# Kernel tuning notes

Hardware: AMD Instinct MI355X
Metric: run time of the kernel (lower is better)

## Reference

```python
import jax, jax.numpy as jnp
import numpy as np

N = 10000      # number of keypoints / graph nodes
CIN = 512      # in_channels
COUT = 512     # out_channels
KCHEB = 5      # Chebyshev order K
KNN = 20       # k nearest neighbors


def setup_inputs() -> dict:
    key = jax.random.key(0)
    k1, k2, k3, k4 = jax.random.split(key, 4)
    x = jax.random.normal(k1, (1, CIN, N), dtype=jnp.float32)
    position = jax.random.normal(k2, (1, N, 3), dtype=jnp.float32)
    # ChebConv weights: one [CIN, COUT] matrix per Chebyshev order, plus bias
    theta = jax.random.normal(k3, (KCHEB, CIN, COUT), dtype=jnp.float32) / np.float32(np.sqrt(CIN * KCHEB))
    bias = jax.random.normal(k4, (COUT,), dtype=jnp.float32) * 0.01
    return {"x": x, "position": position, "theta": theta, "bias": bias, "knn": KNN}


def reference(x, position, theta, bias, knn):
    # ---- knn_graph(position.squeeze(0), k, flow='target_to_source') ----
    pos = position[0]                       # [N, 3]
    n = pos.shape[0]
    sq = jnp.sum(pos * pos, axis=1)
    d2 = sq[:, None] + sq[None, :] - 2.0 * (pos @ pos.T)   # [N, N] squared dists
    d2 = jnp.where(jnp.eye(n, dtype=bool), jnp.inf, d2)    # exclude self (loop=False)
    _, nbr = jax.lax.top_k(-d2, knn)        # [N, knn] nearest neighbor indices
    # flow='target_to_source' => edge_index = [center, neighbor]
    row = jnp.repeat(jnp.arange(n), knn)    # edge source (center) for ChebConv
    col = nbr.reshape(-1)                   # edge target (neighbor)

    # ---- ChebConv sym normalization, lambda_max=2 => L_hat = -D^-1/2 A D^-1/2 ----
    deg = jnp.zeros((n,), x.dtype).at[row].add(jnp.float32(1.0))
    dis = jnp.where(deg > 0, jax.lax.rsqrt(deg), jnp.float32(0.0))
    w = -dis[row] * dis[col]                # [E] edge weights, zero diagonal

    h = jnp.swapaxes(x, 1, 2)               # [B, N, CIN]

    def prop(t):
        # out[target] += w * t[source]  (sparse L_hat @ t)
        msg = t[:, row, :] * w[None, :, None]
        return jnp.zeros_like(t).at[:, col, :].add(msg)

    # Chebyshev recurrence: Tx0 = h, Tx1 = L_hat h, Tx_k = 2 L_hat Tx_{k-1} - Tx_{k-2}
    Tx0 = h
    out = jnp.einsum('bnc,co->bno', Tx0, theta[0])
    Tx1 = prop(Tx0)
    out = out + jnp.einsum('bnc,co->bno', Tx1, theta[1])
    for k in range(2, theta.shape[0]):
        Tx2 = 2.0 * prop(Tx1) - Tx0
        out = out + jnp.einsum('bnc,co->bno', Tx2, theta[k])
        Tx0, Tx1 = Tx1, Tx2
    out = out + bias
    return jnp.swapaxes(out, 1, 2)          # [B, COUT, N]
```

## Files before the change

### kernel.cpp

```cpp
#include <hip/hip_runtime.h>
#include <hip/hip_bf16.h>
#include <cstdint>
#include <cstddef>

#define N_NODES 10000
#define KNN_K 20
#define NEDGE (N_NODES * KNN_K)
#define NBATCH 157
#define POS4_PAD 10048
#define NCELL 4096
#define NPX 1250

using bf16x8 = __attribute__((ext_vector_type(8))) short;
using f32x4  = __attribute__((ext_vector_type(4))) float;

__device__ __forceinline__ float bf_lo(unsigned int u) {
  union { unsigned int i; float f; } c; c.i = u << 16; return c.f;
}
__device__ __forceinline__ float bf_hi(unsigned int u) {
  union { unsigned int i; float f; } c; c.i = u & 0xFFFF0000u; return c.f;
}
__device__ __forceinline__ unsigned short f2bf(float f) {
  union { float f; unsigned int i; } c; c.f = f;
  unsigned int u = c.i;
  u += 0x7FFFu + ((u >> 16) & 1u);
  return (unsigned short)(u >> 16);
}

__device__ __forceinline__ void gll16(const void* g, void* l) {
  __builtin_amdgcn_global_load_lds(
      (const __attribute__((address_space(1))) unsigned int*)g,
      (__attribute__((address_space(3))) unsigned int*)l,
      16, 0, 0);
}

__global__ __launch_bounds__(256) void transpose_f32_bf16(
    const float* __restrict__ src0, unsigned short* __restrict__ dst,
    int srows, int scols, int dstride, size_t slice_elems, int dcol_per_slice)
{
  __shared__ float lds[64 * 65];
  const int z = blockIdx.z;
  const float* src = src0 + (size_t)z * slice_elems;
  const int dcol0 = z * dcol_per_slice;
  const int c0 = blockIdx.x * 64;
  const int r0 = blockIdx.y * 64;
  const int tid = threadIdx.x;
#pragma unroll
  for (int q = 0; q < 4; ++q) {
    int unit = q * 256 + tid;
    int rr = unit >> 4;
    int cu = unit & 15;
    int r = r0 + rr, c = c0 + cu * 4;
    float4 v = make_float4(0.f, 0.f, 0.f, 0.f);
    if (r < srows && c + 3 < scols) v = *(const float4*)&src[(size_t)r * scols + c];
    lds[rr * 65 + cu * 4 + 0] = v.x;
    lds[rr * 65 + cu * 4 + 1] = v.y;
    lds[rr * 65 + cu * 4 + 2] = v.z;
    lds[rr * 65 + cu * 4 + 3] = v.w;
  }
  __syncthreads();
#pragma unroll
  for (int q = 0; q < 2; ++q) {
    int unit = q * 256 + tid;
    int cl = unit >> 3;
    int ru = unit & 7;
    int c = c0 + cl;
    if (c < scols) {
      unsigned short tmp[8];
#pragma unroll
      for (int j = 0; j < 8; ++j) tmp[j] = f2bf(lds[(ru * 8 + j) * 65 + cl]);
      uint4 o;
      o.x = (unsigned int)tmp[0] | ((unsigned int)tmp[1] << 16);
      o.y = (unsigned int)tmp[2] | ((unsigned int)tmp[3] << 16);
      o.z = (unsigned int)tmp[4] | ((unsigned int)tmp[5] << 16);
      o.w = (unsigned int)tmp[6] | ((unsigned int)tmp[7] << 16);
      *(uint4*)&dst[(size_t)c * dstride + dcol0 + r0 + ru * 8] = o;
    }
  }
}

__global__ __launch_bounds__(256) void pos4_kernel(
    const float* __restrict__ pos, float4* __restrict__ pos4,
    int* __restrict__ counts, int* __restrict__ cursor,
    int* __restrict__ cellid, int* __restrict__ cellcnt,
    int* __restrict__ nfail)
{
  int c = blockIdx.x * 256 + threadIdx.x;
  if (c == 0) *nfail = 0;
  if (c < POS4_PAD) {
    float4 v;
    if (c < N_NODES) {
      float x = pos[c * 3 + 0], y = pos[c * 3 + 1], z = pos[c * 3 + 2];
      v = make_float4(x, y, z, x * x + y * y + z * z);
      int cx = min(15, max(0, (int)floorf((x + 4.0f) * 2.0f)));
      int cy = min(15, max(0, (int)floorf((y + 4.0f) * 2.0f)));
      int cz = min(15, max(0, (int)floorf((z + 4.0f) * 2.0f)));
      int cell = (cx << 8) | (cy << 4) | cz;
      cellid[c] = cell;
      atomicAdd(&cellcnt[cell], 1);
      counts[c] = 0; cursor[c] = 0;
    } else {
      v = make_float4(0.f, 0.f, 0.f, __builtin_inff());
    }
    pos4[c] = v;
  }
}

__global__ __launch_bounds__(256) void cellscan_kernel(
    const int* __restrict__ cellcnt, int* __restrict__ cellptr)
{
  __shared__ int part[256];
  const int tid = threadIdx.x;
  const int base = tid * 16;
  int cv[16];
  int s = 0;
#pragma unroll
  for (int q = 0; q < 4; ++q) {
    int4 v = *(const int4*)&cellcnt[base + q * 4];
    cv[q * 4 + 0] = v.x; cv[q * 4 + 1] = v.y;
    cv[q * 4 + 2] = v.z; cv[q * 4 + 3] = v.w;
    s += v.x + v.y + v.z + v.w;
  }
  part[tid] = s;
  __syncthreads();
  for (int off = 1; off < 256; off <<= 1) {
    int add = (tid >= off) ? part[tid - off] : 0;
    __syncthreads();
    part[tid] += add;
    __syncthreads();
  }
  int run = part[tid] - s;
#pragma unroll
  for (int q = 0; q < 16; ++q) { cellptr[base + q] = run; run += cv[q]; }
  if (tid == 255) cellptr[NCELL] = run;
}

__global__ __launch_bounds__(256) void perm_kernel(
    const int* __restrict__ cellid, const int* __restrict__ cellptr,
    int* __restrict__ cellcur, int* __restrict__ perm,
    const float4* __restrict__ pos4, float4* __restrict__ pos4s)
{
  int c = blockIdx.x * 256 + threadIdx.x;
  if (c < N_NODES) {
    int cell = cellid[c];
    int p = atomicAdd(&cellcur[cell], 1);
    int slot = cellptr[cell] + p;
    perm[slot] = c;
    pos4s[slot] = pos4[c];
  }
}

__device__ __forceinline__ float knn_dist(float4 pi, float4 s) {
  float dot = fmaf(pi.x, s.x, fmaf(pi.y, s.y, pi.z * s.z));
  return fmaf(-2.0f, dot, pi.w + s.w);
}

__device__ __forceinline__ void insert8(float r[8], float k) {
  asm("v_med3_f32 %0, %1, %2, %3" : "=v"(r[7]) : "v"(k), "v"(r[6]), "v"(r[7]));
  asm("v_med3_f32 %0, %1, %2, %3" : "=v"(r[6]) : "v"(k), "v"(r[5]), "v"(r[6]));
  asm("v_med3_f32 %0, %1, %2, %3" : "=v"(r[5]) : "v"(k), "v"(r[4]), "v"(r[5]));
  asm("v_med3_f32 %0, %1, %2, %3" : "=v"(r[4]) : "v"(k), "v"(r[3]), "v"(r[4]));
  asm("v_med3_f32 %0, %1, %2, %3" : "=v"(r[3]) : "v"(k), "v"(r[2]), "v"(r[3]));
  asm("v_med3_f32 %0, %1, %2, %3" : "=v"(r[2]) : "v"(k), "v"(r[1]), "v"(r[2]));
  asm("v_med3_f32 %0, %1, %2, %3" : "=v"(r[1]) : "v"(k), "v"(r[0]), "v"(r[1]));
  r[0] = fminf(r[0], k);
}

__device__ __forceinline__ float merge_tau20(float r[8], int lane) {
  const float INF = __builtin_inff();
  float tau = INF;
#pragma unroll
  for (int t = 0; t < KNN_K; ++t) {
    float m = r[0];
    m = fminf(m, __shfl_xor(m, 1));
    m = fminf(m, __shfl_xor(m, 2));
    m = fminf(m, __shfl_xor(m, 4));
    m = fminf(m, __shfl_xor(m, 8));
    m = fminf(m, __shfl_xor(m, 16));
    m = fminf(m, __shfl_xor(m, 32));
    unsigned long long who = __ballot(r[0] == m);
    int srcl = __ffsll(who) - 1;
    if (lane == srcl) {
#pragma unroll
      for (int z = 0; z < 7; ++z) r[z] = r[z + 1];
      r[7] = INF;
    }
    tau = m;
  }
  return tau;
}

__device__ __forceinline__ void emit_hits(
    int i, bool valid, float d, float tau, int cid, int lane, int& cnt,
    int* __restrict__ knn_out)
{
  unsigned long long less = __ballot(valid && d < tau);
  unsigned long long eq   = __ballot(valid && d == tau);
  if (less) {
    if (valid && d < tau) {
      int pos = cnt + (int)__popcll(less & ((1ull << lane) - 1ull));
      if (pos < KNN_K) knn_out[i * KNN_K + pos] = cid;
    }
    cnt += (int)__popcll(less);
  }
  if (eq && cnt < KNN_K) {
    if (valid && d == tau) {
      int pos = cnt + (int)__popcll(eq & ((1ull << lane) - 1ull));
      if (pos < KNN_K) knn_out[i * KNN_K + pos] = cid;
    }
    cnt = min(KNN_K, cnt + (int)__popcll(eq));
  }
}

__global__ __launch_bounds__(256) void knn_try_kernel(
    const float4* __restrict__ pos4, const float4* __restrict__ pos4s,
    const int* __restrict__ perm, const int* __restrict__ cellptr,
    int* __restrict__ knn_out, int* __restrict__ wl, int* __restrict__ nfail)
{
  const int lane = threadIdx.x & 63, wave = threadIdx.x >> 6;
  const int wid = blockIdx.x * 4 + wave;
  const int i = perm[wid];
  const float4 pi = pos4[i];
  const float INF = __builtin_inff();

  const int cx = min(15, max(0, (int)floorf((pi.x + 4.0f) * 2.0f)));
  const int cy = min(15, max(0, (int)floorf((pi.y + 4.0f) * 2.0f)));
  const int cz = min(15, max(0, (int)floorf((pi.z + 4.0f) * 2.0f)));
  const int x0 = max(cx - 1, 0), x1 = min(cx + 1, 15);
  const int y0 = max(cy - 1, 0), y1 = min(cy + 1, 15);
  const int z0 = max(cz - 1, 0), z1 = min(cz + 1, 15);

  float r[8];
#pragma unroll
  for (int q = 0; q < 8; ++q) r[q] = INF;

  for (int X = x0; X <= x1; ++X)
    for (int Y = y0; Y <= y1; ++Y) {
      const int cb = (X << 8) | (Y << 4);
      const int s0 = cellptr[cb + z0], s1 = cellptr[cb + z1 + 1];
      for (int c0 = s0; c0 < s1; c0 += 64) {
        const int slot = c0 + lane;
        const int idx = min(slot, s1 - 1);
        const float4 s = pos4s[idx];
        const int nid = perm[idx];
        float d = knn_dist(pi, s);
        float k = (slot < s1 && nid != i) ? d : INF;
        insert8(r, k);
      }
    }
  float tau = merge_tau20(r, lane);

  float mx = INF, my = INF, mz = INF;
  if (x0 > 0)  mx = pi.x - (x0 * 0.5f - 4.0f);
  if (x1 < 15) mx = fminf(mx, ((x1 + 1) * 0.5f - 4.0f) - pi.x);
  if (y0 > 0)  my = pi.y - (y0 * 0.5f - 4.0f);
  if (y1 < 15) my = fminf(my, ((y1 + 1) * 0.5f - 4.0f) - pi.y);
  if (z0 > 0)  mz = pi.z - (z0 * 0.5f - 4.0f);
  if (z1 < 15) mz = fminf(mz, ((z1 + 1) * 0.5f - 4.0f) - pi.z);
  const float marg = fminf(mx, fminf(my, mz));

  if (tau < marg * marg) {
    int cnt = 0;
    for (int X = x0; X <= x1; ++X)
      for (int Y = y0; Y <= y1; ++Y) {
        const int cb = (X << 8) | (Y << 4);
        const int s0 = cellptr[cb + z0], s1 = cellptr[cb + z1 + 1];
        for (int c0 = s0; c0 < s1; c0 += 64) {
          const int slot = c0 + lane;
          const int idx = min(slot, s1 - 1);
          const float4 s = pos4s[idx];
          const int nid = perm[idx];
          float d = knn_dist(pi, s);
          bool valid = (slot < s1) && (nid != i);
          emit_hits(i, valid, d, tau, nid, lane, cnt, knn_out);
        }
      }
    return;
  }

  if (lane == 0) {
    int slot = atomicAdd(nfail, 1);
    wl[slot] = i;
  }
}

__global__ __launch_bounds__(256) void knn_full_kernel(
    const float4* __restrict__ pos4, const int* __restrict__ wl,
    const int* __restrict__ nfail, int* __restrict__ knn_out)
{
  const int lane = threadIdx.x & 63, wave = threadIdx.x >> 6;
  const int w = blockIdx.x * 4 + wave;
  if (w >= *nfail) return;
  const int i = wl[w];
  const float4 pi = pos4[i];
  const float INF = __builtin_inff();

  float r[8];
#pragma unroll
  for (int q = 0; q < 8; ++q) r[q] = INF;
#pragma unroll 4
  for (int b = 0; b < NBATCH; ++b) {
    const int cid = b * 64 + lane;
    const float4 s = pos4[cid];
    float d = knn_dist(pi, s);
    float k = (cid == i) ? INF : d;
    insert8(r, k);
  }
  float tau = merge_tau20(r, lane);
  int cnt = 0;
  for (int b = 0; b < NBATCH; ++b) {
    const int cid = b * 64 + lane;
    const float4 s = pos4[cid];
    float d = knn_dist(pi, s);
    bool valid = (cid != i);
    emit_hits(i, valid, d, tau, cid, lane, cnt, knn_out);
  }
}

__global__ __launch_bounds__(256) void count_kernel(
    const int* __restrict__ knn, int* __restrict__ counts)
{
  int e = blockIdx.x * 256 + threadIdx.x;
  if (e < NEDGE) atomicAdd(&counts[knn[e]], 1);
}

__global__ __launch_bounds__(256) void scan_kernel(
    const int* __restrict__ counts, int* __restrict__ rptr)
{
  __shared__ int part[256];
  const int tid = threadIdx.x;
  const int base = tid * 40;
  int s = 0;
  int cv[40];
  if (tid < 250) {
#pragma unroll
    for (int q = 0; q < 10; ++q) {
      int4 v = *(const int4*)&counts[base + q * 4];
      cv[q * 4 + 0] = v.x; cv[q * 4 + 1] = v.y;
      cv[q * 4 + 2] = v.z; cv[q * 4 + 3] = v.w;
      s += v.x + v.y + v.z + v.w;
    }
  }
  part[tid] = s;
  __syncthreads();
  for (int off = 1; off < 256; off <<= 1) {
    int add = (tid >= off) ? part[tid - off] : 0;
    __syncthreads();
    part[tid] += add;
    __syncthreads();
  }
  int run = part[tid] - s;
  if (tid < 250) {
#pragma unroll
    for (int q = 0; q < 40; ++q) { rptr[base + q] = run; run += cv[q]; }
  }
  if (tid == 255) rptr[N_NODES] = run;
}

__global__ __launch_bounds__(256) void fill_kernel(
    const int* __restrict__ knn, const int* __restrict__ rptr,
    int* __restrict__ cursor, int* __restrict__ rsrc)
{
  int e = blockIdx.x * 256 + threadIdx.x;
  if (e < NEDGE) {
    int j = knn[e];
    int i = e / KNN_K;
    int p = atomicAdd(&cursor[j], 1);
    rsrc[rptr[j] + p] = i;
  }
}

__global__ __launch_bounds__(256) void sort_kernel(
    const int* __restrict__ rptr, int* __restrict__ rsrc)
{
  const int lane = threadIdx.x & 63, wave = threadIdx.x >> 6;
  const int j = blockIdx.x * 4 + wave;
  const int s0 = rptr[j], s1 = rptr[j + 1], deg = s1 - s0;
  if (deg <= 64) {
    int v = (lane < deg) ? rsrc[s0 + lane] : 0x7FFFFFFF;
#pragma unroll
    for (int k = 2; k <= 64; k <<= 1) {
#pragma unroll
      for (int m = k >> 1; m > 0; m >>= 1) {
        int other = __shfl_xor(v, m);
        bool up = ((lane & k) == 0);
        bool lower = ((lane & m) == 0);
        v = (up == lower) ? min(v, other) : max(v, other);
      }
    }
    if (lane < deg) rsrc[s0 + lane] = v;
  } else if (lane == 0) {
    for (int a = s0 + 1; a < s1; ++a) {
      int v = rsrc[a];
      int b = a - 1;
      while (b >= s0 && rsrc[b] > v) { rsrc[b + 1] = rsrc[b]; --b; }
      rsrc[b + 1] = v;
    }
  }
}

__global__ __launch_bounds__(256) void prop_kernel(
    const unsigned short* __restrict__ tin, const unsigned short* __restrict__ tprev,
    unsigned short* __restrict__ tout, const int* __restrict__ rptr,
    const int* __restrict__ rsrc, const int* __restrict__ perm, float scale2)
{
  const int wave = threadIdx.x >> 6, lane = threadIdx.x & 63;
  const int b = blockIdx.x;
  const int xcd = b & 7, qb = b >> 3;
  const int local = qb * 4 + wave;
  if (local >= NPX) return;
  const int j = perm[xcd * NPX + local];
  const int s0 = rptr[j], s1 = rptr[j + 1];
  const size_t coff = (size_t)lane * 8;

  float a0[8], a1[8], a2[8], a3[8];
#pragma unroll
  for (int q = 0; q < 8; ++q) { a0[q] = 0.f; a1[q] = 0.f; a2[q] = 0.f; a3[q] = 0.f; }

  for (int base = s0; base < s1; base += 64) {
    const int clen = min(64, s1 - base);
    int myidx = (base + lane < s1) ? rsrc[base + lane] : 0;
    int t = 0;
    for (; t + 4 <= clen; t += 4) {
      int i0 = __shfl(myidx, t);
      int i1 = __shfl(myidx, t + 1);
      int i2 = __shfl(myidx, t + 2);
      int i3 = __shfl(myidx, t + 3);
      uint4 v0 = *(const uint4*)&tin[(size_t)i0 * 512 + coff];
      uint4 v1 = *(const uint4*)&tin[(size_t)i1 * 512 + coff];
      uint4 v2 = *(const uint4*)&tin[(size_t)i2 * 512 + coff];
      uint4 v3 = *(const uint4*)&tin[(size_t)i3 * 512 + coff];
      a0[0] += bf_lo(v0.x); a0[1] += bf_hi(v0.x); a0[2] += bf_lo(v0.y); a0[3] += bf_hi(v0.y);
      a0[4] += bf_lo(v0.z); a0[5] += bf_hi(v0.z); a0[6] += bf_lo(v0.w); a0[7] += bf_hi(v0.w);
      a1[0] += bf_lo(v1.x); a1[1] += bf_hi(v1.x); a1[2] += bf_lo(v1.y); a1[3] += bf_hi(v1.y);
      a1[4] += bf_lo(v1.z); a1[5] += bf_hi(v1.z); a1[6] += bf_lo(v1.w); a1[7] += bf_hi(v1.w);
      a2[0] += bf_lo(v2.x); a2[1] += bf_hi(v2.x); a2[2] += bf_lo(v2.y); a2[3] += bf_hi(v2.y);
      a2[4] += bf_lo(v2.z); a2[5] += bf_hi(v2.z); a2[6] += bf_lo(v2.w); a2[7] += bf_hi(v2.w);
      a3[0] += bf_lo(v3.x); a3[1] += bf_hi(v3.x); a3[2] += bf_lo(v3.y); a3[3] += bf_hi(v3.y);
      a3[4] += bf_lo(v3.z); a3[5] += bf_hi(v3.z); a3[6] += bf_lo(v3.w); a3[7] += bf_hi(v3.w);
    }
    for (; t < clen; ++t) {
      int i0 = __shfl(myidx, t);
      uint4 v0 = *(const uint4*)&tin[(size_t)i0 * 512 + coff];
      a0[0] += bf_lo(v0.x); a0[1] += bf_hi(v0.x); a0[2] += bf_lo(v0.y); a0[3] += bf_hi(v0.y);
      a0[4] += bf_lo(v0.z); a0[5] += bf_hi(v0.z); a0[6] += bf_lo(v0.w); a0[7] += bf_hi(v0.w);
    }
  }

  float pv[8] = {0.f, 0.f, 0.f, 0.f, 0.f, 0.f, 0.f, 0.f};
  if (tprev != nullptr) {
    uint4 p = *(const uint4*)&tprev[(size_t)j * 512 + coff];
    pv[0] = bf_lo(p.x); pv[1] = bf_hi(p.x);
    pv[2] = bf_lo(p.y); pv[3] = bf_hi(p.y);
    pv[4] = bf_lo(p.z); pv[5] = bf_hi(p.z);
    pv[6] = bf_lo(p.w); pv[7] = bf_hi(p.w);
  }
  unsigned short o16[8];
#pragma unroll
  for (int q = 0; q < 8; ++q) {
    float acc = (a0[q] + a1[q]) + (a2[q] + a3[q]);
    o16[q] = f2bf(scale2 * acc - pv[q]);
  }
  uint4 o;
  o.x = (unsigned int)o16[0] | ((unsigned int)o16[1] << 16);
  o.y = (unsigned int)o16[2] | ((unsigned int)o16[3] << 16);
  o.z = (unsigned int)o16[4] | ((unsigned int)o16[5] << 16);
  o.w = (unsigned int)o16[6] | ((unsigned int)o16[7] << 16);
  *(uint4*)&tout[(size_t)j * 512 + coff] = o;
}

__global__ __launch_bounds__(256) void gemm_kernel(
    const unsigned short* __restrict__ A,
    const unsigned short* __restrict__ Bt,
    const float* __restrict__ bias,
    float* __restrict__ C)
{
  __shared__ __align__(16) char smem[64 * 132 * 4];
  unsigned short* As = (unsigned short*)smem;
  unsigned short* Bs = As + 128 * 64;
  float* eps = (float*)smem;

  const int tid = threadIdx.x;
  const int wave = tid >> 6, lane = tid & 63;
  const int l15 = lane & 15, hi = lane >> 4;
  const int wr = wave >> 1, wc = wave & 1;
  const int n0 = blockIdx.x * 128;
  const int o0 = blockIdx.y * 128;

  f32x4 acc[4][4];
#pragma unroll
  for (int a = 0; a < 4; ++a)
#pragma unroll
    for (int b = 0; b < 4; ++b) acc[a][b] = (f32x4){0.f, 0.f, 0.f, 0.f};

  for (int kt = 0; kt < 40; ++kt) {
    const int k0 = kt * 64;
    const int ko = k0 >> 9;
    const int c0 = k0 & 511;
    const unsigned short* Ab = A + (size_t)ko * ((size_t)N_NODES * 512);
#pragma unroll
    for (int q = 0; q < 4; ++q) {
      int idx = (wave * 4 + q) * 64 + lane;
      int r = idx >> 3, u = idx & 7;
      gll16(Ab + (size_t)(n0 + r) * 512 + c0 + u * 8, As + (size_t)(wave * 4 + q) * 512);
    }
#pragma unroll
    for (int q = 0; q < 4; ++q) {
      int idx = (wave * 4 + q) * 64 + lane;
      int r = idx >> 3, u = idx & 7;
      gll16(Bt + (size_t)(o0 + r) * 2560 + k0 + u * 8, Bs + (size_t)(wave * 4 + q) * 512);
    }
    __syncthreads();
#pragma unroll
    for (int kk = 0; kk < 2; ++kk) {
      bf16x8 af[4], bfr[4];
#pragma unroll
      for (int mi = 0; mi < 4; ++mi)
        af[mi] = *(const bf16x8*)(As + ((wr * 64 + mi * 16 + l15) * 64 + kk * 32 + hi * 8));
#pragma unroll
      for (int ni = 0; ni < 4; ++ni)
        bfr[ni] = *(const bf16x8*)(Bs + ((wc * 64 + ni * 16 + l15) * 64 + kk * 32 + hi * 8));
#pragma unroll
      for (int mi = 0; mi < 4; ++mi)
#pragma unroll
        for (int ni = 0; ni < 4; ++ni)
          acc[mi][ni] = __builtin_amdgcn_mfma_f32_16x16x32_bf16(af[mi], bfr[ni], acc[mi][ni], 0, 0, 0);
    }
    __syncthreads();
  }

#pragma unroll
  for (int h = 0; h < 2; ++h) {
    __syncthreads();
    if (wc == h) {
#pragma unroll
      for (int mi = 0; mi < 4; ++mi)
#pragma unroll
        for (int ni = 0; ni < 4; ++ni) {
          int o_l = ni * 16 + l15;
          int nb = wr * 64 + mi * 16 + hi * 4;
          *(f32x4*)&eps[o_l * 132 + nb] = acc[mi][ni];
        }
    }
    __syncthreads();
#pragma unroll
    for (int q = 0; q < 8; ++q) {
      int unit = q * 256 + tid;
      int o_l = unit >> 5, nu = unit & 31;
      int n = n0 + nu * 4;
      if (n < N_NODES) {
        int o = o0 + h * 64 + o_l;
        f32x4 v = *(const f32x4*)&eps[o_l * 132 + nu * 4];
        float bo = bias[o];
        v = v + bo;
        *(f32x4*)&C[(size_t)o * N_NODES + n] = v;
      }
    }
  }
}

extern "C" void kernel_launch(void* const* d_in, const int* in_sizes, int n_in,
                              void* d_out, int out_size, void* d_ws, size_t ws_size,
                              hipStream_t stream)
{
  const float* x        = (const float*)d_in[0];
  const float* position = (const float*)d_in[1];
  const float* theta    = (const float*)d_in[2];
  const float* bias     = (const float*)d_in[3];

  char* ws = (char*)d_ws;
  size_t off = 0;
  auto alloc = [&](size_t bytes) -> void* {
    void* p = ws + off;
    off = (off + bytes + 255) & ~(size_t)255;
    return p;
  };
  unsigned short* TxAll   = (unsigned short*)alloc(5ull * N_NODES * 512 * 2 + 131072);
  unsigned short* thetabT = (unsigned short*)alloc(512ull * 2560 * 2);
  float4* pos4  = (float4*)alloc((size_t)POS4_PAD * 16);
  float4* pos4s = (float4*)alloc((size_t)N_NODES * 16);
  int* knn    = (int*)alloc((size_t)NEDGE * 4);
  int* rptr   = (int*)alloc((size_t)(N_NODES + 1) * 4);
  int* counts = (int*)alloc((size_t)N_NODES * 4);
  int* cursor = (int*)alloc((size_t)N_NODES * 4);
  int* rsrc   = (int*)alloc((size_t)NEDGE * 4);
  int* cellcnt = (int*)alloc((size_t)NCELL * 4);
  int* cellcur = (int*)alloc((size_t)NCELL * 4);
  int* cellptr = (int*)alloc((size_t)(NCELL + 1) * 4);
  int* cellid  = (int*)alloc((size_t)N_NODES * 4);
  int* perm    = (int*)alloc((size_t)N_NODES * 4);
  int* wl      = (int*)alloc((size_t)N_NODES * 4);
  int* nfail   = (int*)alloc(256);
  if (ws_size < off) return;

  transpose_f32_bf16<<<dim3(8, 8, 5), 256, 0, stream>>>(
      theta, thetabT, 512, 512, 2560, (size_t)512 * 512, 512);
  transpose_f32_bf16<<<dim3(157, 8, 1), 256, 0, stream>>>(
      x, TxAll, 512, N_NODES, 512, 0, 0);

  hipMemsetAsync(cellcnt, 0, (size_t)((char*)cellptr - (char*)cellcnt), stream);
  pos4_kernel<<<40, 256, 0, stream>>>(position, pos4, counts, cursor, cellid, cellcnt, nfail);
  cellscan_kernel<<<1, 256, 0, stream>>>(cellcnt, cellptr);
  perm_kernel<<<40, 256, 0, stream>>>(cellid, cellptr, cellcur, perm, pos4, pos4s);

  knn_try_kernel<<<2500, 256, 0, stream>>>(pos4, pos4s, perm, cellptr, knn, wl, nfail);
  knn_full_kernel<<<2500, 256, 0, stream>>>(pos4, wl, nfail, knn);

  count_kernel<<<(NEDGE + 255) / 256, 256, 0, stream>>>(knn, counts);
  scan_kernel<<<1, 256, 0, stream>>>(counts, rptr);
  fill_kernel<<<(NEDGE + 255) / 256, 256, 0, stream>>>(knn, rptr, cursor, rsrc);
  sort_kernel<<<2500, 256, 0, stream>>>(rptr, rsrc);

  unsigned short* Tx0 = TxAll;
  unsigned short* Tx1 = TxAll + 1ull * N_NODES * 512;
  unsigned short* Tx2 = TxAll + 2ull * N_NODES * 512;
  unsigned short* Tx3 = TxAll + 3ull * N_NODES * 512;
  unsigned short* Tx4 = TxAll + 4ull * N_NODES * 512;

  prop_kernel<<<2504, 256, 0, stream>>>(Tx0, nullptr, Tx1, rptr, rsrc, perm, -0.05f);
  prop_kernel<<<2504, 256, 0, stream>>>(Tx1, Tx0,     Tx2, rptr, rsrc, perm, -0.10f);
  prop_kernel<<<2504, 256, 0, stream>>>(Tx2, Tx1,     Tx3, rptr, rsrc, perm, -0.10f);
  prop_kernel<<<2504, 256, 0, stream>>>(Tx3, Tx2,     Tx4, rptr, rsrc, perm, -0.10f);

  gemm_kernel<<<dim3(79, 4), 256, 0, stream>>>(TxAll, thetabT, bias, (float*)d_out);
}
```

Before: 268.1 us.

## Double-buffer GEMM LDS tiles, swizzle layout, and remap blocks per XCD

The GEMM kernel now keeps two LDS stages so the next K-tile's global-to-LDS loads are issued while the current tile's MFMAs run. This removes the sync-then-wait stall at each iteration. LDS rows are XOR-swizzled to avoid bank conflicts on the fragment reads. Blocks are remapped so that neighbouring tiles land on the same XCD, which should improve L2 reuse of the A and B tiles. The cost is 64KB of LDS per block, which lowers occupancy, plus a few idle padded blocks.

Measured after the change: 249.1 us. 7.1% less time.

```diff
diff --git a/kernel.cpp b/kernel.cpp
--- a/kernel.cpp
+++ b/kernel.cpp
@@ -10,6 +10,7 @@
 #define POS4_PAD 10048
 #define NCELL 4096
 #define NPX 1250
+#define GM_PAIRS 316
 
 using bf16x8 = __attribute__((ext_vector_type(8))) short;
 using f32x4  = __attribute__((ext_vector_type(4))) float;
@@ -475,17 +476,23 @@
     const float* __restrict__ bias,
     float* __restrict__ C)
 {
-  __shared__ __align__(16) char smem[64 * 132 * 4];
-  unsigned short* As = (unsigned short*)smem;
-  unsigned short* Bs = As + 128 * 64;
+  __shared__ __align__(16) char smem[65536];
   float* eps = (float*)smem;
 
   const int tid = threadIdx.x;
   const int wave = tid >> 6, lane = tid & 63;
   const int l15 = lane & 15, hi = lane >> 4;
   const int wr = wave >> 1, wc = wave & 1;
-  const int n0 = blockIdx.x * 128;
-  const int o0 = blockIdx.y * 128;
+
+  const int bid = blockIdx.x;
+  const int xcd = bid & 7, local = bid >> 3;
+  const int qd = GM_PAIRS >> 3, rem = GM_PAIRS & 7;
+  const int cnt = (xcd < rem) ? qd + 1 : qd;
+  if (local >= cnt) return;
+  const int start = (xcd < rem) ? xcd * (qd + 1) : rem * (qd + 1) + (xcd - rem) * qd;
+  const int pair = start + local;
+  const int n0 = (pair >> 2) * 128;
+  const int o0 = (pair & 3) * 128;
 
   f32x4 acc[4][4];
 #pragma unroll
@@ -493,33 +500,52 @@
 #pragma unroll
     for (int b = 0; b < 4; ++b) acc[a][b] = (f32x4){0.f, 0.f, 0.f, 0.f};
 
-  for (int kt = 0; kt < 40; ++kt) {
+  auto stage = [&](int kt, int sel) {
     const int k0 = kt * 64;
     const int ko = k0 >> 9;
     const int c0 = k0 & 511;
     const unsigned short* Ab = A + (size_t)ko * ((size_t)N_NODES * 512);
+    unsigned short* As = (unsigned short*)(smem + sel * 32768);
+    unsigned short* Bs = As + 128 * 64;
 #pragma unroll
     for (int q = 0; q < 4; ++q) {
       int idx = (wave * 4 + q) * 64 + lane;
       int r = idx >> 3, u = idx & 7;
-      gll16(Ab + (size_t)(n0 + r) * 512 + c0 + u * 8, As + (size_t)(wave * 4 + q) * 512);
+      int ug = u ^ (r & 7);
+      gll16(Ab + (size_t)(n0 + r) * 512 + c0 + ug * 8, As + (size_t)(wave * 4 + q) * 512);
     }
 #pragma unroll
     for (int q = 0; q < 4; ++q) {
       int idx = (wave * 4 + q) * 64 + lane;
       int r = idx >> 3, u = idx & 7;
-      gll16(Bt + (size_t)(o0 + r) * 2560 + k0 + u * 8, Bs + (size_t)(wave * 4 + q) * 512);
-    }
-    __syncthreads();
+      int ug = u ^ (r & 7);
+      gll16(Bt + (size_t)(o0 + r) * 2560 + k0 + ug * 8, Bs + (size_t)(wave * 4 + q) * 512);
+    }
+  };
+
+  stage(0, 0);
+  __syncthreads();
+
+  int cur = 0;
+  for (int kt = 0; kt < 40; ++kt) {
+    if (kt + 1 < 40) stage(kt + 1, cur ^ 1);
+    unsigned short* As = (unsigned short*)(smem + cur * 32768);
+    unsigned short* Bs = As + 128 * 64;
 #pragma unroll
     for (int kk = 0; kk < 2; ++kk) {
       bf16x8 af[4], bfr[4];
 #pragma unroll
-      for (int mi = 0; mi < 4; ++mi)
-        af[mi] = *(const bf16x8*)(As + ((wr * 64 + mi * 16 + l15) * 64 + kk * 32 + hi * 8));
-#pragma unroll
-      for (int ni = 0; ni < 4; ++ni)
-        bfr[ni] = *(const bf16x8*)(Bs + ((wc * 64 + ni * 16 + l15) * 64 + kk * 32 + hi * 8));
+      for (int mi = 0; mi < 4; ++mi) {
+        int row = wr * 64 + mi * 16 + l15;
+        int up = (kk * 4 + hi) ^ (row & 7);
+        af[mi] = *(const bf16x8*)(As + row * 64 + up * 8);
+      }
+#pragma unroll
+      for (int ni = 0; ni < 4; ++ni) {
+        int row = wc * 64 + ni * 16 + l15;
+        int up = (kk * 4 + hi) ^ (row & 7);
+        bfr[ni] = *(const bf16x8*)(Bs + row * 64 + up * 8);
+      }
 #pragma unroll
       for (int mi = 0; mi < 4; ++mi)
 #pragma unroll
@@ -527,6 +553,7 @@
           acc[mi][ni] = __builtin_amdgcn_mfma_f32_16x16x32_bf16(af[mi], bfr[ni], acc[mi][ni], 0, 0, 0);
     }
     __syncthreads();
+    cur ^= 1;
   }
 
 #pragma unroll
@@ -622,5 +649,5 @@
   prop_kernel<<<2504, 256, 0, stream>>>(Tx2, Tx1,     Tx3, rptr, rsrc, perm, -0.10f);
   prop_kernel<<<2504, 256, 0, stream>>>(Tx3, Tx2,     Tx4, rptr, rsrc, perm, -0.10f);
 
-  gemm_kernel<<<dim3(79, 4), 256, 0, stream>>>(TxAll, thetabT, bias, (float*)d_out);
-}
+  gemm_kernel<<<320, 256, 0, stream>>>(TxAll, thetabT, bias, (float*)d_out);
+}
```
